# Performance work log

Measured on AMD Instinct MI355X. Metric: run time of the kernel, lower is better.

The kernel has to match this reference:

```python
import jax, jax.numpy as jnp
import numpy as np

EMBED_DIM = 1024
HEAD_DIM = 64


def setup_inputs() -> dict:
    key = jax.random.key(0)
    k1, k2, k3, k4 = jax.random.split(key, 4)
    B, T = 4, 4096
    x = jax.random.normal(k1, (B, T, EMBED_DIM), dtype=jnp.float32)
    # nn.Linear(EMBED_DIM, head_dim, bias=False): store as (EMBED_DIM, head_dim)
    s = (1.0 / np.sqrt(EMBED_DIM)).astype(np.float32)
    Wk = jax.random.uniform(k2, (EMBED_DIM, HEAD_DIM), jnp.float32, -s, s)
    Wq = jax.random.uniform(k3, (EMBED_DIM, HEAD_DIM), jnp.float32, -s, s)
    Wv = jax.random.uniform(k4, (EMBED_DIM, HEAD_DIM), jnp.float32, -s, s)
    return {"x": x, "Wq": Wq, "Wk": Wk, "Wv": Wv}


def reference(x, Wq, Wk, Wv):
    B, T, E = x.shape
    q = jnp.einsum('bte,ed->btd', x, Wq)  # (B,T,D)
    k = jnp.einsum('bte,ed->btd', x, Wk)
    v = jnp.einsum('bte,ed->btd', x, Wv)
    # NOTE: original scales by EMBED_DIM**-0.5 (x.size(-1)), not head_dim**-0.5
    scale = jnp.asarray(E, x.dtype) ** -0.5
    scores = jnp.einsum('bqd,bkd->bqk', q, k) * scale  # (B,T,T)
    causal = jnp.tril(jnp.ones((T, T), dtype=bool))
    scores = jnp.where(causal, scores, jnp.asarray(-jnp.inf, scores.dtype))
    attn = jax.nn.softmax(scores, axis=-1)
    # dropout is identity at inference (deterministic baseline)
    out = jnp.einsum('bqk,bkd->bqd', attn, v)  # (B,T,D)
    return out
```

## Files before the change

### kernel.cpp

```cpp
#include <hip/hip_runtime.h>
#include <hip/hip_bf16.h>
#include <stdint.h>

#define BATCH 4
#define SEQ   4096
#define EMB   1024
#define HD    64

typedef __bf16 bf16x8 __attribute__((ext_vector_type(8)));
typedef float  f32x4  __attribute__((ext_vector_type(4)));
typedef float  f32x16 __attribute__((ext_vector_type(16)));
typedef unsigned u32x2v __attribute__((ext_vector_type(2)));
typedef unsigned short u16;

#define QSCALE 0.04508422002777948f

__device__ __forceinline__ u16 f2bf(float f) {
    union { __bf16 h; u16 u; } c; c.h = (__bf16)f; return c.u;
}
__device__ __forceinline__ unsigned pk2(float lo, float hi) {
    union { __bf16 e[2]; unsigned u; } c;
    c.e[0] = (__bf16)lo; c.e[1] = (__bf16)hi; return c.u;
}
__device__ __forceinline__ void gld16(const void* g, void* l) {
    __builtin_amdgcn_global_load_lds(
        (const __attribute__((address_space(1))) void*)g,
        (__attribute__((address_space(3))) void*)l, 16, 0, 0);
}
__device__ __forceinline__ void halfswap(unsigned &a, unsigned &b) {
#if __has_builtin(__builtin_amdgcn_permlane32_swap)
    u32x2v r = __builtin_amdgcn_permlane32_swap(a, b, false, false);
    a = r.x; b = r.y;
#else
    const unsigned pa = (unsigned)__shfl_xor((int)a, 32);
    const unsigned pb = (unsigned)__shfl_xor((int)b, 32);
    const bool hi = (threadIdx.x & 32) != 0;
    const unsigned na = hi ? pb : a;
    const unsigned nb = hi ? b : pa;
    a = na; b = nb;
#endif
}

__global__ __launch_bounds__(256) void wt_kernel(
        const float* __restrict__ Wq, const float* __restrict__ Wk,
        const float* __restrict__ Wv, u16* __restrict__ Wt) {
    int idx = blockIdx.x * 256 + threadIdx.x;
    int i = idx >> 16;
    int r = idx & 65535;
    int n = r >> 10;
    int k = r & 1023;
    const float* W = (i == 0) ? Wq : (i == 1) ? Wk : Wv;
    Wt[idx] = f2bf(W[k * HD + n]);
}

__global__ __launch_bounds__(256) void qkv_kernel(
        const float* __restrict__ x, const u16* __restrict__ Wt,
        u16* __restrict__ Qw, u16* __restrict__ Kw, u16* __restrict__ Vt) {
    __shared__ float xs[2][2048];
    __shared__ u16   wsb[2][12288];

    const int t    = threadIdx.x;
    const int wave = t >> 6;
    const int lane = t & 63;
    const int m16  = lane & 15;
    const int quad = lane >> 4;
    const int rh   = wave & 1;
    const int ch   = wave >> 1;
    const int R0   = blockIdx.x * 32;

    #define ISSUE(buf_, kt_) do {                                              \
        const int r4_ = lane >> 4, c16_ = lane & 15;                           \
        _Pragma("unroll")                                                      \
        for (int j_ = 0; j_ < 2; ++j_) {                                       \
            const int ii_  = wave + (j_ << 2);                                 \
            const int row_ = (ii_ << 2) + r4_;                      \
            const int kc_  = c16_ ^ (row_ & 15);                               \
            gld16(x + (size_t)(R0 + row_) * EMB + ((kt_) << 6) + (kc_ << 2),   \
                  &xs[buf_][ii_ << 8]);                                        \
        }                                                                      \
        const int r8_ = lane >> 3, c8_ = lane & 7;                             \
        _Pragma("unroll")                                                      \
        for (int j_ = 0; j_ < 6; ++j_) {                                       \
            const int rb_ = (wave * 6 + j_) << 3;                  \
            const int kw_ = c8_ ^ r8_;                                         \
            gld16(Wt + (size_t)(rb_ + r8_) * 1024 + ((kt_) << 6) + (kw_ << 3), \
                  &wsb[buf_][(wave * 6 + j_) << 9]);                           \
        }                                                                      \
    } while (0)

    f32x4 acc[6];
#pragma unroll
    for (int a = 0; a < 6; ++a) acc[a] = (f32x4){0.f, 0.f, 0.f, 0.f};

    const int row_x = rh * 16 + m16;
    ISSUE(0, 0);

    for (int kt = 0; kt < 16; ++kt) {
        const int buf = kt & 1;
        __syncthreads();
        if (kt < 15) ISSUE(buf ^ 1, kt + 1);

#pragma unroll
        for (int ks2 = 0; ks2 < 2; ++ks2) {
            const int c0 = (ks2 << 3) + (quad << 1);
            const float4 a0 = *(const float4*)&xs[buf][(row_x << 6) + ((c0 ^ m16) << 2)];
            const float4 a1 = *(const float4*)&xs[buf][(row_x << 6) + (((c0 + 1) ^ m16) << 2)];
            union { bf16x8 v; __bf16 e[8]; } af;
            af.e[0] = (__bf16)a0.x; af.e[1] = (__bf16)a0.y;
            af.e[2] = (__bf16)a0.z; af.e[3] = (__bf16)a0.w;
            af.e[4] = (__bf16)a1.x; af.e[5] = (__bf16)a1.y;
            af.e[6] = (__bf16)a1.z; af.e[7] = (__bf16)a1.w;
#pragma unroll
            for (int i = 0; i < 6; ++i) {
                const int tt   = ch * 6 + i;
                const int rowW = (tt << 4) + m16;
                const bf16x8 bf = *(const bf16x8*)&wsb[buf][
                        (rowW << 6) + ((((ks2 << 2) + quad) ^ (m16 & 7)) << 3)];
                acc[i] = __builtin_amdgcn_mfma_f32_16x16x32_bf16(af.v, bf, acc[i], 0, 0, 0);
            }
        }
    }
    #undef ISSUE

    const int rowbase = R0 + rh * 16 + (quad << 2);
    const int bidx = rowbase >> 12;
    const int t0   = rowbase & 4095;
#pragma unroll
    for (int i = 0; i < 6; ++i) {
        const int tt  = ch * 6 + i;
        const int w3  = tt >> 2;
        const int col = ((tt & 3) << 4) + m16;
        if (w3 == 0) {
#pragma unroll
            for (int reg = 0; reg < 4; ++reg)
                Qw[(size_t)(rowbase + reg) * HD + col] = f2bf(acc[i][reg] * QSCALE);
        } else if (w3 == 1) {
#pragma unroll
            for (int reg = 0; reg < 4; ++reg)
                Kw[(size_t)(rowbase + reg) * HD + col] = f2bf(acc[i][reg]);
        } else {
            union { ushort4 vv; __bf16 e[4]; } o;
            o.e[0] = (__bf16)acc[i][0]; o.e[1] = (__bf16)acc[i][1];
            o.e[2] = (__bf16)acc[i][2]; o.e[3] = (__bf16)acc[i][3];
            *(ushort4*)(Vt + (size_t)((bidx << 6) + col) * SEQ + t0) = o.vv;
        }
    }
}

__global__ __launch_bounds__(256, 4) void attn_part_kernel(
        const u16* __restrict__ Qw, const u16* __restrict__ Kw,
        const u16* __restrict__ Vt, float* __restrict__ Opart,
        float* __restrict__ Mp, float* __restrict__ Lp) {
    __shared__ u16 kv[2][2][4096];

    const int pid = blockIdx.x;
    const int c   = pid >> 7;
    const int i   = pid & 127;
    const int b   = i & 3;
    const int hq  = i >> 2;
    const int qt  = hq ^ (int)((0x071817080F101F00ULL >> (c * 8)) & 31u);
    const int part = (((b << 5) + qt) << 3) + c;
    const int jmax = 2 * qt + 1;

    const int wave = threadIdx.x >> 6;
    const int lane = threadIdx.x & 63;
    const int l31  = lane & 31;
    const int h    = lane >> 5;

    #define ISSUE_KV(buf_, jt_) do {                                           \
        const int r8_ = lane >> 3, c8_ = lane & 7;                             \
        const int kc_ = c8_ ^ r8_;                                             \
        _Pragma("unroll")                                                      \
        for (int j_ = 0; j_ < 2; ++j_) {                                       \
            const int row_ = ((wave * 2 + j_) << 3) + r8_;          \
            gld16(Kw + ((size_t)(b * SEQ + ((jt_) << 6) + row_) << 6) + (kc_ << 3), \
                  &kv[buf_][0][(wave * 2 + j_) << 9]);                         \
            gld16(Vt + (size_t)((b << 6) + row_) * SEQ + ((jt_) << 6) + (kc_ << 3), \
                  &kv[buf_][1][(wave * 2 + j_) << 9]);                         \
        }                                                                      \
    } while (0)

    const int qg = (qt << 7) + (wave << 5) + l31;
    const u16* qbase = Qw + ((size_t)(b * SEQ + qg) << 6);
    bf16x8 qf[4];
#pragma unroll
    for (int s = 0; s < 4; ++s)
        qf[s] = *(const bf16x8*)(qbase + (s << 4) + (h << 3));

    f32x16 o[2];
#pragma unroll
    for (int dt = 0; dt < 2; ++dt)
#pragma unroll
        for (int k = 0; k < 16; ++k) o[dt][k] = 0.f;
    float m_i = -3.0e38f, l_i = 0.f;
    const int qmin_w = (qt << 7) + (wave << 5);

    if (c <= jmax) ISSUE_KV(0, c);

    int buf = 0;
    for (int jt = c; jt <= jmax; jt += 8) {
        __syncthreads();
        if (jt + 8 <= jmax) ISSUE_KV(buf ^ 1, jt + 8);

        if ((jt << 6) <= qmin_w + 31) {
            f32x16 s2[2];
#pragma unroll
            for (int mt = 0; mt < 2; ++mt) {
                f32x16 sa;
#pragma unroll
                for (int k = 0; k < 16; ++k) sa[k] = 0.f;
                const int row = (mt << 5) + l31;
                const int rb  = row << 6;
                const int rx  = row & 7;
#pragma unroll
                for (int s = 0; s < 4; ++s) {
                    const bf16x8 kf = *(const bf16x8*)&kv[buf][0][
                            rb + ((((s << 1) + h) ^ rx) << 3)];
                    sa = __builtin_amdgcn_mfma_f32_32x32x16_bf16(kf, qf[s], sa, 0, 0, 0);
                }
                s2[mt] = sa;
            }

            if ((jt << 6) + 63 > qmin_w) {
#pragma unroll
                for (int mt = 0; mt < 2; ++mt)
#pragma unroll
                for (int reg = 0; reg < 16; ++reg) {
                    const int kg = (jt << 6) + (mt << 5) +
                                   (reg & 3) + ((reg >> 2) << 3) + (h << 2);
                    if (kg > qg) s2[mt][reg] = -3.0e38f;
                }
            }

            float tm = s2[0][0];
#pragma unroll
            for (int mt = 0; mt < 2; ++mt)
#pragma unroll
            for (int reg = 0; reg < 16; ++reg) tm = fmaxf(tm, s2[mt][reg]);
            tm = fmaxf(tm, __shfl_xor(tm, 32));

            if (__any(tm > m_i + 8.0f)) {
                const float mnew = fmaxf(m_i, tm);
                const float al = __builtin_amdgcn_exp2f(m_i - mnew);
                m_i = mnew; l_i *= al;
#pragma unroll
                for (int dt = 0; dt < 2; ++dt)
#pragma unroll
                for (int k = 0; k < 16; ++k) o[dt][k] *= al;
            }

            float ps = 0.f;
#pragma unroll
            for (int mt = 0; mt < 2; ++mt)
#pragma unroll
            for (int reg = 0; reg < 16; ++reg) {
                const float p = __builtin_amdgcn_exp2f(s2[mt][reg] - m_i);
                s2[mt][reg] = p; ps += p;
            }
            l_i += ps;

            union F { unsigned d[4]; bf16x8 v; } pf[4];
#pragma unroll
            for (int mt = 0; mt < 2; ++mt) {
                unsigned A0 = pk2(s2[mt][0],  s2[mt][1]);
                unsigned B0 = pk2(s2[mt][4],  s2[mt][5]);
                unsigned C0 = pk2(s2[mt][2],  s2[mt][3]);
                unsigned D0 = pk2(s2[mt][6],  s2[mt][7]);
                halfswap(A0, B0); halfswap(C0, D0);
                pf[2*mt].d[0] = A0; pf[2*mt].d[1] = C0;
                pf[2*mt].d[2] = B0; pf[2*mt].d[3] = D0;
                unsigned A1 = pk2(s2[mt][8],  s2[mt][9]);
                unsigned B1 = pk2(s2[mt][12], s2[mt][13]);
                unsigned C1 = pk2(s2[mt][10], s2[mt][11]);
                unsigned D1 = pk2(s2[mt][14], s2[mt][15]);
                halfswap(A1, B1); halfswap(C1, D1);
                pf[2*mt+1].d[0] = A1; pf[2*mt+1].d[1] = C1;
                pf[2*mt+1].d[2] = B1; pf[2*mt+1].d[3] = D1;
            }

#pragma unroll
            for (int dt = 0; dt < 2; ++dt) {
                const int row = (dt << 5) + l31;
                const int rb  = row << 6;
                const int rx  = row & 7;
                f32x16 oa = o[dt];
#pragma unroll
                for (int s = 0; s < 4; ++s) {
                    const bf16x8 vf = *(const bf16x8*)&kv[buf][1][
                            rb + ((((s << 1) + h) ^ rx) << 3)];
                    oa = __builtin_amdgcn_mfma_f32_32x32x16_bf16(vf, pf[s].v, oa, 0, 0, 0);
                }
                o[dt] = oa;
            }
        }
        buf ^= 1;
    }
    #undef ISSUE_KV

    const float l2 = l_i + __shfl_xor(l_i, 32);

    float* ob = Opart + ((size_t)part << 13) + (wave << 5) + l31;
#pragma unroll
    for (int dt = 0; dt < 2; ++dt)
#pragma unroll
    for (int reg = 0; reg < 16; ++reg) {
        const int d = (dt << 5) + (reg & 3) + ((reg >> 2) << 3) + (h << 2);
        ob[d << 7] = o[dt][reg];
    }
    if (lane < 32) {
        Mp[part * 128 + (wave << 5) + l31] = m_i;
        Lp[part * 128 + (wave << 5) + l31] = l2;
    }
}

__global__ __launch_bounds__(256) void combine_kernel(
        const float* __restrict__ Opart, const float* __restrict__ Mp,
        const float* __restrict__ Lp, float* __restrict__ out) {
    const int gb = blockIdx.x;
    const int bq = gb >> 1;
    const int qh = gb & 1;
    const int t  = threadIdx.x;
    const int ql = (qh << 6) + (t & 63);
    const int d0 = (t >> 6) << 4;
    const int pb = bq << 3;

    float mv[8];
    float M = -3.0e38f;
#pragma unroll
    for (int cc = 0; cc < 8; ++cc) {
        mv[cc] = Mp[(pb + cc) * 128 + ql];
        M = fmaxf(M, mv[cc]);
    }
    float o16[16];
#pragma unroll
    for (int k = 0; k < 16; ++k) o16[k] = 0.f;
    float den = 0.f;
#pragma unroll
    for (int cc = 0; cc < 8; ++cc) {
        const float w = __builtin_amdgcn_exp2f(mv[cc] - M);
        den += w * Lp[(pb + cc) * 128 + ql];
        const float* op = Opart + ((size_t)(pb + cc) << 13) + ql;
#pragma unroll
        for (int k = 0; k < 16; ++k)
            o16[k] = fmaf(w, op[(d0 + k) << 7], o16[k]);
    }
    const float rd = 1.0f / den;
    float* orow = out + (((size_t)bq << 7) + ql) * 64 + d0;
#pragma unroll
    for (int j = 0; j < 4; ++j) {
        float4 v;
        v.x = o16[4*j]     * rd; v.y = o16[4*j + 1] * rd;
        v.z = o16[4*j + 2] * rd; v.w = o16[4*j + 3] * rd;
        *(float4*)(orow + 4*j) = v;
    }
}

extern "C" void kernel_launch(void* const* d_in, const int* in_sizes, int n_in,
                              void* d_out, int out_size, void* d_ws, size_t ws_size,
                              hipStream_t stream) {
    const float* x  = (const float*)d_in[0];
    const float* Wq = (const float*)d_in[1];
    const float* Wk = (const float*)d_in[2];
    const float* Wv = (const float*)d_in[3];
    float* out = (float*)d_out;

    char* ws = (char*)d_ws;
    u16* Qw     = (u16*)(ws);
    u16* Kw     = (u16*)(ws + (2u << 20));
    u16* Vt     = (u16*)(ws + (4u << 20));
    u16* Wt     = (u16*)(ws + (6u << 20));
    float* Opart = (float*)(ws + (8u << 20));
    float* Mp   = (float*)(ws + (40u << 20));
    float* Lp   = (float*)(ws + (40u << 20) + (512u << 10));

    wt_kernel<<<768, 256, 0, stream>>>(Wq, Wk, Wv, Wt);
    qkv_kernel<<<512, 256, 0, stream>>>(x, Wt, Qw, Kw, Vt);
    attn_part_kernel<<<1024, 256, 0, stream>>>(Qw, Kw, Vt, Opart, Mp, Lp);
    combine_kernel<<<256, 256, 0, stream>>>(Opart, Mp, Lp, out);
}
```

Baseline: 143.4 us.

## Fuse split-KV combine into attention kernel via last-block atomic counter

Removes the separate combine kernel launch. Each attention block bumps an atomic counter per (batch, query-tile), and the eighth block to finish merges all partial outputs for that tile. Partial outputs are also stored as bf16 instead of fp32, which halves their write and read traffic. In exchange it adds threadfence and atomic overhead, puts the serial combine work on the tail blocks, and loses some precision in the partial accumulators.

```diff
diff --git a/kernel.cpp b/kernel.cpp
--- a/kernel.cpp
+++ b/kernel.cpp
@@ -17,6 +17,10 @@
 
 __device__ __forceinline__ u16 f2bf(float f) {
     union { __bf16 h; u16 u; } c; c.h = (__bf16)f; return c.u;
+}
+__device__ __forceinline__ float bf2f(u16 h) {
+    union { uint32_t u; float f; } cv; cv.u = ((uint32_t)h) << 16;
+    return cv.f;
 }
 __device__ __forceinline__ unsigned pk2(float lo, float hi) {
     union { __bf16 e[2]; unsigned u; } c;
@@ -43,8 +47,10 @@
 
 __global__ __launch_bounds__(256) void wt_kernel(
         const float* __restrict__ Wq, const float* __restrict__ Wk,
-        const float* __restrict__ Wv, u16* __restrict__ Wt) {
+        const float* __restrict__ Wv, u16* __restrict__ Wt,
+        int* __restrict__ cnt) {
     int idx = blockIdx.x * 256 + threadIdx.x;
+    if (idx < 128) cnt[idx] = 0;
     int i = idx >> 16;
     int r = idx & 65535;
     int n = r >> 10;
@@ -149,9 +155,11 @@
 
 __global__ __launch_bounds__(256, 4) void attn_part_kernel(
         const u16* __restrict__ Qw, const u16* __restrict__ Kw,
-        const u16* __restrict__ Vt, float* __restrict__ Opart,
-        float* __restrict__ Mp, float* __restrict__ Lp) {
+        const u16* __restrict__ Vt, u16* __restrict__ Opart,
+        float* __restrict__ Mp, float* __restrict__ Lp,
+        float* __restrict__ out, int* __restrict__ cnt) {
     __shared__ u16 kv[2][2][4096];
+    __shared__ int sdone;
 
     const int pid = blockIdx.x;
     const int c   = pid >> 7;
@@ -159,7 +167,8 @@
     const int b   = i & 3;
     const int hq  = i >> 2;
     const int qt  = hq ^ (int)((0x071817080F101F00ULL >> (c * 8)) & 31u);
-    const int part = (((b << 5) + qt) << 3) + c;
+    const int bq  = (b << 5) + qt;
+    const int part = (bq << 3) + c;
     const int jmax = 2 * qt + 1;
 
     const int wave = threadIdx.x >> 6;
@@ -299,59 +308,60 @@
 
     const float l2 = l_i + __shfl_xor(l_i, 32);
 
-    float* ob = Opart + ((size_t)part << 13) + (wave << 5) + l31;
+    u16* ob = Opart + ((size_t)part << 13) + (wave << 5) + l31;
 #pragma unroll
     for (int dt = 0; dt < 2; ++dt)
 #pragma unroll
     for (int reg = 0; reg < 16; ++reg) {
         const int d = (dt << 5) + (reg & 3) + ((reg >> 2) << 3) + (h << 2);
-        ob[d << 7] = o[dt][reg];
+        ob[d << 7] = f2bf(o[dt][reg]);
     }
     if (lane < 32) {
         Mp[part * 128 + (wave << 5) + l31] = m_i;
         Lp[part * 128 + (wave << 5) + l31] = l2;
     }
-}
-
-__global__ __launch_bounds__(256) void combine_kernel(
-        const float* __restrict__ Opart, const float* __restrict__ Mp,
-        const float* __restrict__ Lp, float* __restrict__ out) {
-    const int gb = blockIdx.x;
-    const int bq = gb >> 1;
-    const int qh = gb & 1;
-    const int t  = threadIdx.x;
-    const int ql = (qh << 6) + (t & 63);
-    const int d0 = (t >> 6) << 4;
-    const int pb = bq << 3;
-
-    float mv[8];
-    float M = -3.0e38f;
-#pragma unroll
-    for (int cc = 0; cc < 8; ++cc) {
-        mv[cc] = Mp[(pb + cc) * 128 + ql];
-        M = fmaxf(M, mv[cc]);
-    }
-    float o16[16];
-#pragma unroll
-    for (int k = 0; k < 16; ++k) o16[k] = 0.f;
-    float den = 0.f;
-#pragma unroll
-    for (int cc = 0; cc < 8; ++cc) {
-        const float w = __builtin_amdgcn_exp2f(mv[cc] - M);
-        den += w * Lp[(pb + cc) * 128 + ql];
-        const float* op = Opart + ((size_t)(pb + cc) << 13) + ql;
-#pragma unroll
-        for (int k = 0; k < 16; ++k)
-            o16[k] = fmaf(w, op[(d0 + k) << 7], o16[k]);
-    }
-    const float rd = 1.0f / den;
-    float* orow = out + (((size_t)bq << 7) + ql) * 64 + d0;
-#pragma unroll
-    for (int j = 0; j < 4; ++j) {
-        float4 v;
-        v.x = o16[4*j]     * rd; v.y = o16[4*j + 1] * rd;
-        v.z = o16[4*j + 2] * rd; v.w = o16[4*j + 3] * rd;
-        *(float4*)(orow + 4*j) = v;
+
+    __threadfence();
+    if (threadIdx.x == 0) sdone = atomicAdd(&cnt[bq], 1);
+    __syncthreads();
+    if (sdone == 7) {
+        __threadfence();
+        const int t  = threadIdx.x;
+        const int pb = bq << 3;
+        const int d0 = (t >> 6) << 4;
+#pragma unroll
+        for (int qh = 0; qh < 2; ++qh) {
+            const int ql = (qh << 6) + (t & 63);
+            float mv[8];
+            float M = -3.0e38f;
+#pragma unroll
+            for (int cc = 0; cc < 8; ++cc) {
+                mv[cc] = Mp[(pb + cc) * 128 + ql];
+                M = fmaxf(M, mv[cc]);
+            }
+            float o16[16];
+#pragma unroll
+            for (int k = 0; k < 16; ++k) o16[k] = 0.f;
+            float den = 0.f;
+#pragma unroll
+            for (int cc = 0; cc < 8; ++cc) {
+                const float w = __builtin_amdgcn_exp2f(mv[cc] - M);
+                den += w * Lp[(pb + cc) * 128 + ql];
+                const u16* op = Opart + ((size_t)(pb + cc) << 13) + ql;
+#pragma unroll
+                for (int k = 0; k < 16; ++k)
+                    o16[k] = fmaf(w, bf2f(op[(d0 + k) << 7]), o16[k]);
+            }
+            const float rd = 1.0f / den;
+            float* orow = out + (((size_t)bq << 7) + ql) * 64 + d0;
+#pragma unroll
+            for (int j = 0; j < 4; ++j) {
+                float4 v;
+                v.x = o16[4*j]     * rd; v.y = o16[4*j + 1] * rd;
+                v.z = o16[4*j + 2] * rd; v.w = o16[4*j + 3] * rd;
+                *(float4*)(orow + 4*j) = v;
+            }
+        }
     }
 }
 
@@ -369,12 +379,12 @@
     u16* Kw     = (u16*)(ws + (2u << 20));
     u16* Vt     = (u16*)(ws + (4u << 20));
     u16* Wt     = (u16*)(ws + (6u << 20));
-    float* Opart = (float*)(ws + (8u << 20));
-    float* Mp   = (float*)(ws + (40u << 20));
-    float* Lp   = (float*)(ws + (40u << 20) + (512u << 10));
-
-    wt_kernel<<<768, 256, 0, stream>>>(Wq, Wk, Wv, Wt);
+    u16* Opart  = (u16*)(ws + (8u << 20));
+    float* Mp   = (float*)(ws + (24u << 20));
+    float* Lp   = (float*)(ws + (24u << 20) + (512u << 10));
+    int*   cnt  = (int*)(ws + (25u << 20));
+
+    wt_kernel<<<768, 256, 0, stream>>>(Wq, Wk, Wv, Wt, cnt);
     qkv_kernel<<<512, 256, 0, stream>>>(x, Wt, Qw, Kw, Vt);
-    attn_part_kernel<<<1024, 256, 0, stream>>>(Qw, Kw, Vt, Opart, Mp, Lp);
-    combine_kernel<<<256, 256, 0, stream>>>(Opart, Mp, Lp, out);
-}
+    attn_part_kernel<<<1024, 256, 0, stream>>>(Qw, Kw, Vt, Opart, Mp, Lp, out, cnt);
+}
```

After: 282.3 us. 1.97x slower.
